# Kernel tuning notes

Hardware: AMD Instinct MI355X
Metric: run time of the kernel (lower is better)

Reference implementation:

```python
import jax, jax.numpy as jnp
import numpy as np

BATCH, IN, HID, OUT = 4096, 1024, 2048, 1000
ITERS = 50
LR = 0.001


def setup_inputs() -> dict:
    key = jax.random.key(0)
    k1, k2, k3 = jax.random.split(key, 3)
    x = jax.random.uniform(k1, (BATCH, IN), dtype=jnp.float32)
    # xavier_uniform for W_rec [HID, IN] and W_out [OUT, HID]
    lim_rec = float(np.sqrt(6.0 / (HID + IN)))
    lim_out = float(np.sqrt(6.0 / (OUT + HID)))
    W_rec = jax.random.uniform(k2, (HID, IN), minval=-lim_rec, maxval=lim_rec, dtype=jnp.float32)
    W_out = jax.random.uniform(k3, (OUT, HID), minval=-lim_out, maxval=lim_out, dtype=jnp.float32)
    bias_out = jnp.zeros((OUT,), dtype=jnp.float32)
    bias_gen = jnp.zeros((IN,), dtype=jnp.float32)
    return {"x": x, "W_rec": W_rec, "W_out": W_out, "bias_out": bias_out, "bias_gen": bias_gen}


def reference(x, W_rec, W_out, bias_out, bias_gen):
    batch = x.shape[0]
    h0 = jnp.zeros((batch, HID), dtype=x.dtype)
    y0 = jnp.zeros((batch, OUT), dtype=x.dtype)

    def step(carry, _):
        h, y, total_e = carry
        # generative prediction of input: sigmoid(h @ W_rec + bias_gen) [B, IN]
        x_pred = jax.nn.sigmoid(jnp.matmul(h, W_rec) + bias_gen)
        e_x = x - x_pred
        h = h + LR * jnp.matmul(e_x, W_rec.T)          # [B, HID]
        y_pred = jnp.matmul(h, W_out.T) + bias_out     # [B, OUT]
        e_y = y - y_pred
        y = y + LR * e_y
        energy = jnp.mean(jnp.sum(e_x * e_x, axis=1)) + jnp.mean(jnp.sum(e_y * e_y, axis=1))
        return (h, y, total_e + energy), None

    (h, y, total_energy), _ = jax.lax.scan(step, (h0, y0, jnp.float32(0.0)), None, length=ITERS)
    average_energy = total_energy / ITERS
    return y, average_energy
```

## Files before the change

### kernel.cpp

```cpp
#include <hip/hip_runtime.h>
#include <hip/hip_bf16.h>
#include <cstdint>

typedef __bf16 bf16_t;
typedef __bf16 bf16x4 __attribute__((ext_vector_type(4)));
typedef __bf16 bf16x8 __attribute__((ext_vector_type(8)));
typedef float f32x4 __attribute__((ext_vector_type(4)));

#define BATCH 4096
#define DIN   1024
#define HID   2048
#define DOUT  1000
#define NITER 50
#define LR    0.001f

#define BM 128
#define BN 128
#define BK 32
#define NBUF 4

#define GLDS(g, l)                                                        \
    __builtin_amdgcn_global_load_lds(                                     \
        (const __attribute__((address_space(1))) void*)(g),               \
        (__attribute__((address_space(3))) void*)(l), 16, 0, 0)

#define WAITVM(N) asm volatile("s_waitcnt vmcnt(" #N ")" ::: "memory")
#define BAR()     __builtin_amdgcn_s_barrier()
#define SCHEDB()  __builtin_amdgcn_sched_barrier(0)

template <int MODE>
__global__ __launch_bounds__(512) void pc_gemm(
    const bf16_t* __restrict__ Aex, bf16_t* __restrict__ wrecT,
    bf16_t* __restrict__ woutP, bf16_t* __restrict__ wg,
    bf16_t* __restrict__ wc,
    const float* __restrict__ xin, const float* __restrict__ bias_g,
    const float* __restrict__ bias_o,
    bf16_t* __restrict__ exnext, float* __restrict__ u,
    float* __restrict__ z, bf16_t* __restrict__ ey,
    float* __restrict__ yout, float* __restrict__ energy)
{
    __shared__ __align__(16) bf16_t sA[NBUF][BM * BK];
    __shared__ __align__(16) bf16_t sB[NBUF][BN * BK];
    __shared__ float red[8];

    const int t    = threadIdx.x;
    const int lane = t & 63;
    const int wave = t >> 6;
    const int wm   = wave >> 2;
    const int wn   = wave & 3;
    const int m0   = blockIdx.x * BM;
    const int lr   = lane & 15;
    const int lkb  = (lane >> 4) * 8;

    int role, n0, K;
    const bf16_t *Aop, *Bop;
    if constexpr (MODE == 3) {
        role = (int)blockIdx.y >= 8; n0 = ((int)blockIdx.y & 7) * BN; K = HID;
        Aop = role ? woutP : wrecT;  Bop = wrecT;
    } else if constexpr (MODE == 2) {
        role = 1; n0 = (int)blockIdx.y * BN; K = DIN;
        Aop = Aex; Bop = wc;
    } else {
        role = (int)blockIdx.y >= 8; n0 = ((int)blockIdx.y & 7) * BN; K = DIN;
        Aop = Aex; Bop = role ? wc : wg;
    }

    f32x4 acc[4][2] = {};

    const int srow = wave * 16 + (lane >> 2);
    const int scol = (lane & 3) * 8;
    const bf16_t* gA = Aop + (int64_t)(m0 + srow) * K + scol;
    const bf16_t* gB = Bop + (int64_t)(n0 + srow) * K + scol;

    auto stage = [&](int tile, int buf) {
        const int64_t ko = (int64_t)tile * BK;
        GLDS(gA + ko, &sA[buf][wave * 512]);
        GLDS(gB + ko, &sB[buf][wave * 512]);
    };

    auto compute = [&](int buf) {
        bf16x8 af[4], bfr[2];
#pragma unroll
        for (int mi = 0; mi < 4; ++mi)
            af[mi] = *reinterpret_cast<const bf16x8*>(
                &sA[buf][(wm * 64 + mi * 16 + lr) * BK + lkb]);
#pragma unroll
        for (int ni = 0; ni < 2; ++ni)
            bfr[ni] = *reinterpret_cast<const bf16x8*>(
                &sB[buf][(wn * 32 + ni * 16 + lr) * BK + lkb]);
#pragma unroll
        for (int mi = 0; mi < 4; ++mi)
#pragma unroll
            for (int ni = 0; ni < 2; ++ni)
                acc[mi][ni] = __builtin_amdgcn_mfma_f32_16x16x32_bf16(
                    af[mi], bfr[ni], acc[mi][ni], 0, 0, 0);
    };

    const int npairs = (K / BK) / 2;
    stage(0, 0); stage(1, 1); stage(2, 2); stage(3, 3);

    for (int p = 0; p < npairs - 2; ++p) {
        const int t0 = 2 * p;
        WAITVM(4);
        BAR();
        SCHEDB();
        compute(t0 & 3);
        compute((t0 + 1) & 3);
        BAR();
        stage(t0 + 4, t0 & 3);
        stage(t0 + 5, (t0 + 1) & 3);
    }
    {
        const int t0 = 2 * npairs - 4;
        WAITVM(4); BAR(); SCHEDB();
        compute(t0 & 3); compute((t0 + 1) & 3);
    }
    {
        const int t0 = 2 * npairs - 2;
        WAITVM(0); BAR(); SCHEDB();
        compute(t0 & 3); compute((t0 + 1) & 3);
    }

    float esum = 0.0f;
    const int prow = (lane >> 4) * 4;
#pragma unroll
    for (int mi = 0; mi < 4; ++mi) {
#pragma unroll
        for (int ni = 0; ni < 2; ++ni) {
            const int col = n0 + wn * 32 + ni * 16 + lr;
#pragma unroll
            for (int j = 0; j < 4; ++j) {
                const int row = m0 + wm * 64 + mi * 16 + prow + j;
                const float v = acc[mi][ni][j];
                if constexpr (MODE == 3) {
                    bf16_t* cout = role ? wc : wg;
                    cout[(int64_t)row * 1024 + col] = (bf16_t)v;
                } else {
                    if (role == 0) {
                        const int64_t idx = (int64_t)row * DIN + col;
                        const float D  = LR * v;
                        const float un = (MODE == 1 ? bias_g[col] : u[idx]) + D;
                        u[idx] = un;
                        const float xp = 1.0f / (1.0f + __expf(-un));
                        const float e  = xin[idx] - xp;
                        exnext[idx] = (bf16_t)e;
                        esum += e * e;
                    } else if (col < DOUT) {
                        const int64_t idx = (int64_t)row * 1024 + col;
                        const float D  = LR * v;
                        const float zn = (MODE == 1 ? bias_o[col] : z[idx]) + D;
                        const float eyn = (MODE == 1)
                            ? -zn
                            : (1.0f + LR) * (float)ey[idx] - D;
                        if constexpr (MODE == 2) {
                            yout[(int64_t)row * DOUT + col] =
                                (1.0f + LR) * eyn + zn;
                        } else {
                            z[idx]  = zn;
                            ey[idx] = (bf16_t)eyn;
                        }
                        esum += eyn * eyn;
                    }
                }
            }
        }
    }
    if constexpr (MODE != 3) {
#pragma unroll
        for (int off = 32; off; off >>= 1) esum += __shfl_down(esum, off, 64);
        if (lane == 0) red[wave] = esum;
        __syncthreads();
        if (t == 0) {
            float s = 0.0f;
#pragma unroll
            for (int w = 0; w < 8; ++w) s += red[w];
            atomicAdd(energy, s);
        }
    }
}

__global__ void conv_wrec(const float* __restrict__ W, bf16_t* __restrict__ WbT)
{
    __shared__ float tile[32][33];
    const int tx = threadIdx.x & 31;
    const int ty = threadIdx.x >> 5;
    const int c0 = blockIdx.x * 32;
    const int r0 = blockIdx.y * 32;
#pragma unroll
    for (int rr = ty; rr < 32; rr += 8)
        tile[rr][tx] = W[(int64_t)(r0 + rr) * DIN + c0 + tx];
    __syncthreads();
#pragma unroll
    for (int rr = ty; rr < 32; rr += 8)
        WbT[(int64_t)(c0 + rr) * HID + r0 + tx] = (bf16_t)tile[tx][rr];
}

__global__ void conv_wout(const float* __restrict__ W, bf16_t* __restrict__ Wb)
{
    const int i = blockIdx.x * 256 + threadIdx.x;
    const int r = i >> 11;
    const int c = i & 2047;
    Wb[i] = (r < DOUT) ? (bf16_t)W[(int64_t)r * HID + c] : (bf16_t)0.0f;
}

__global__ void ex0_kernel(const float* __restrict__ x,
                           const float* __restrict__ bias_g,
                           bf16_t* __restrict__ ex, float* __restrict__ energy)
{
    __shared__ float red[4];
    const int t = threadIdx.x, lane = t & 63, wave = t >> 6;
    const int i = (blockIdx.x * 256 + t) * 4;
    const int c0 = i & (DIN - 1);
    const float4 v = *reinterpret_cast<const float4*>(&x[i]);
    float e[4];
    const float b0 = bias_g[c0], b1 = bias_g[c0 + 1],
                b2 = bias_g[c0 + 2], b3 = bias_g[c0 + 3];
    e[0] = v.x - 1.0f / (1.0f + __expf(-b0));
    e[1] = v.y - 1.0f / (1.0f + __expf(-b1));
    e[2] = v.z - 1.0f / (1.0f + __expf(-b2));
    e[3] = v.w - 1.0f / (1.0f + __expf(-b3));
    bf16x4 o = {(bf16_t)e[0], (bf16_t)e[1], (bf16_t)e[2], (bf16_t)e[3]};
    *reinterpret_cast<bf16x4*>(&ex[i]) = o;
    float esum = e[0]*e[0] + e[1]*e[1] + e[2]*e[2] + e[3]*e[3];
#pragma unroll
    for (int off = 32; off; off >>= 1) esum += __shfl_down(esum, off, 64);
    if (lane == 0) red[wave] = esum;
    __syncthreads();
    if (t == 0) atomicAdd(energy, red[0] + red[1] + red[2] + red[3]);
}

__global__ void finalize_kernel(const float* __restrict__ energy,
                                float* __restrict__ out)
{
    out[0] = energy[0] * (1.0f / ((float)BATCH * (float)NITER));
}

extern "C" void kernel_launch(void* const* d_in, const int* in_sizes, int n_in,
                              void* d_out, int out_size, void* d_ws, size_t ws_size,
                              hipStream_t stream)
{
    (void)in_sizes; (void)n_in; (void)out_size; (void)ws_size;
    const float* x        = (const float*)d_in[0];
    const float* W_rec    = (const float*)d_in[1];
    const float* W_out    = (const float*)d_in[2];
    const float* bias_out = (const float*)d_in[3];
    const float* bias_gen = (const float*)d_in[4];
    float* y = (float*)d_out;

    char* ws = (char*)d_ws;
    size_t off = 0;
    float* u      = (float*)(ws + off);   off += (size_t)BATCH * DIN * 4;
    float* z      = (float*)(ws + off);   off += (size_t)BATCH * 1024 * 4;
    bf16_t* exA   = (bf16_t*)(ws + off);  off += (size_t)BATCH * DIN * 2;
    bf16_t* exB   = (bf16_t*)(ws + off);  off += (size_t)BATCH * DIN * 2;
    bf16_t* ey    = (bf16_t*)(ws + off);  off += (size_t)BATCH * 1024 * 2;
    bf16_t* wrecT = (bf16_t*)(ws + off);  off += (size_t)DIN * HID * 2;
    bf16_t* woutP = (bf16_t*)(ws + off);  off += (size_t)1024 * HID * 2;
    bf16_t* wg    = (bf16_t*)(ws + off);  off += (size_t)1024 * 1024 * 2;
    bf16_t* wc    = (bf16_t*)(ws + off);  off += (size_t)1024 * 1024 * 2;
    float* energy = (float*)(ws + off);   off += 256;

    hipMemsetAsync(energy, 0, 4, stream);

    conv_wrec<<<dim3(DIN / 32, HID / 32), 256, 0, stream>>>(W_rec, wrecT);
    conv_wout<<<(1024 * HID) / 256, 256, 0, stream>>>(W_out, woutP);
    pc_gemm<3><<<dim3(8, 16), 512, 0, stream>>>(
        nullptr, wrecT, woutP, wg, wc, nullptr, nullptr, nullptr,
        nullptr, nullptr, nullptr, nullptr, nullptr, nullptr);

    ex0_kernel<<<(BATCH * DIN) / 1024, 256, 0, stream>>>(x, bias_gen, exA, energy);

    bf16_t* exbuf[2] = {exA, exB};
    for (int it = 0; it < NITER; ++it) {
        const bf16_t* src = exbuf[it & 1];
        bf16_t* dst = exbuf[(it & 1) ^ 1];
        if (it == 0)
            pc_gemm<1><<<dim3(BATCH / BM, 16), 512, 0, stream>>>(
                src, nullptr, nullptr, wg, wc, x, bias_gen, bias_out,
                dst, u, z, ey, nullptr, energy);
        else if (it < NITER - 1)
            pc_gemm<0><<<dim3(BATCH / BM, 16), 512, 0, stream>>>(
                src, nullptr, nullptr, wg, wc, x, bias_gen, bias_out,
                dst, u, z, ey, nullptr, energy);
        else
            pc_gemm<2><<<dim3(BATCH / BM, 8), 512, 0, stream>>>(
                src, nullptr, nullptr, wg, wc, x, bias_gen, bias_out,
                nullptr, u, z, ey, y, energy);
    }
    finalize_kernel<<<1, 1, 0, stream>>>(energy, y + (size_t)BATCH * DOUT);
}
```

Baseline: 2.020 ms.

## Fuse all iterations into one persistent kernel with per-row-block barriers

```diff
diff --git a/kernel.cpp b/kernel.cpp
--- a/kernel.cpp
+++ b/kernel.cpp
@@ -28,20 +28,197 @@
 #define BAR()     __builtin_amdgcn_s_barrier()
 #define SCHEDB()  __builtin_amdgcn_sched_barrier(0)
 
-template <int MODE>
-__global__ __launch_bounds__(512) void pc_gemm(
-    const bf16_t* __restrict__ Aex, bf16_t* __restrict__ wrecT,
-    bf16_t* __restrict__ woutP, bf16_t* __restrict__ wg,
-    bf16_t* __restrict__ wc,
+__device__ __forceinline__ unsigned int bf16_bits(float f) {
+    bf16_t h = (bf16_t)f;
+    unsigned short s;
+    __builtin_memcpy(&s, &h, 2);
+    return (unsigned int)s;
+}
+__device__ __forceinline__ float bf16_val(unsigned short s) {
+    unsigned int u = (unsigned int)s << 16;
+    float f;
+    __builtin_memcpy(&f, &u, 4);
+    return f;
+}
+
+__global__ __launch_bounds__(512, 2) void pc_persist(
+    bf16_t* __restrict__ exA, bf16_t* __restrict__ exB,
+    const bf16_t* __restrict__ wg, const bf16_t* __restrict__ wc,
     const float* __restrict__ xin, const float* __restrict__ bias_g,
     const float* __restrict__ bias_o,
-    bf16_t* __restrict__ exnext, float* __restrict__ u,
-    float* __restrict__ z, bf16_t* __restrict__ ey,
-    float* __restrict__ yout, float* __restrict__ energy)
+    float* __restrict__ yout, float* __restrict__ energy,
+    unsigned int* __restrict__ barcnt)
+{
+    __shared__ __align__(16) bf16_t sA [NBUF][BM * BK];
+    __shared__ __align__(16) bf16_t sBU[NBUF][BN * BK];
+    __shared__ __align__(16) bf16_t sBZ[NBUF][BN * BK];
+    __shared__ float red[8];
+
+    const int t    = threadIdx.x;
+    const int lane = t & 63;
+    const int wave = t >> 6;
+    const int wm   = wave >> 2;
+    const int wn   = wave & 3;
+    const int m    = blockIdx.x >> 3;
+    const int n    = blockIdx.x & 7;
+    const int m0   = m * BM;
+    const int n0   = n * BN;
+    const int lr   = lane & 15;
+    const int lkb  = (lane >> 4) * 8;
+    const int prow = (lane >> 4) * 4;
+
+    const int srow = wave * 16 + (lane >> 2);
+    const int scol = (lane & 3) * 8;
+    const bf16_t* gBu = wg + (int64_t)(n0 + srow) * DIN + scol;
+    const bf16_t* gBz = wc + (int64_t)(n0 + srow) * DIN + scol;
+
+    float uSt[4][2][4];
+    float zSt[4][2][4];
+    unsigned int eyp[4][2][2];
+    float esum = 0.0f;
+
+    const bf16_t* Asrc = exA;
+    bf16_t*       Adst = exB;
+
+    for (int it = 0; it < NITER; ++it) {
+        const bf16_t* gA = Asrc + (int64_t)(m0 + srow) * DIN + scol;
+        f32x4 accU[4][2] = {};
+        f32x4 accZ[4][2] = {};
+
+        auto stage = [&](int tile, int buf) {
+            const int64_t ko = (int64_t)tile * BK;
+            GLDS(gA  + ko, &sA [buf][wave * 512]);
+            GLDS(gBu + ko, &sBU[buf][wave * 512]);
+            GLDS(gBz + ko, &sBZ[buf][wave * 512]);
+        };
+        auto compute = [&](int buf) {
+            bf16x8 af[4], bu[2], bz[2];
+#pragma unroll
+            for (int mi = 0; mi < 4; ++mi)
+                af[mi] = *reinterpret_cast<const bf16x8*>(
+                    &sA[buf][(wm * 64 + mi * 16 + lr) * BK + lkb]);
+#pragma unroll
+            for (int ni = 0; ni < 2; ++ni) {
+                bu[ni] = *reinterpret_cast<const bf16x8*>(
+                    &sBU[buf][(wn * 32 + ni * 16 + lr) * BK + lkb]);
+                bz[ni] = *reinterpret_cast<const bf16x8*>(
+                    &sBZ[buf][(wn * 32 + ni * 16 + lr) * BK + lkb]);
+            }
+#pragma unroll
+            for (int mi = 0; mi < 4; ++mi)
+#pragma unroll
+                for (int ni = 0; ni < 2; ++ni) {
+                    accU[mi][ni] = __builtin_amdgcn_mfma_f32_16x16x32_bf16(
+                        af[mi], bu[ni], accU[mi][ni], 0, 0, 0);
+                    accZ[mi][ni] = __builtin_amdgcn_mfma_f32_16x16x32_bf16(
+                        af[mi], bz[ni], accZ[mi][ni], 0, 0, 0);
+                }
+        };
+
+        const int npairs = (DIN / BK) / 2;
+        stage(0, 0); stage(1, 1); stage(2, 2); stage(3, 3);
+        for (int p = 0; p < npairs - 2; ++p) {
+            const int t0 = 2 * p;
+            WAITVM(6);
+            BAR();
+            SCHEDB();
+            compute(t0 & 3);
+            compute((t0 + 1) & 3);
+            BAR();
+            stage(t0 + 4, t0 & 3);
+            stage(t0 + 5, (t0 + 1) & 3);
+        }
+        {
+            const int t0 = 2 * npairs - 4;
+            WAITVM(6); BAR(); SCHEDB();
+            compute(t0 & 3); compute((t0 + 1) & 3);
+        }
+        {
+            const int t0 = 2 * npairs - 2;
+            WAITVM(0); BAR(); SCHEDB();
+            compute(t0 & 3); compute((t0 + 1) & 3);
+        }
+
+#pragma unroll
+        for (int mi = 0; mi < 4; ++mi) {
+#pragma unroll
+            for (int ni = 0; ni < 2; ++ni) {
+                const int col = n0 + wn * 32 + ni * 16 + lr;
+#pragma unroll
+                for (int j = 0; j < 4; ++j) {
+                    const int row = m0 + wm * 64 + mi * 16 + prow + j;
+                    if (it != NITER - 1) {
+                        const int64_t idx = (int64_t)row * DIN + col;
+                        const float D = LR * accU[mi][ni][j];
+                        const float base = (it == 0) ? bias_g[col]
+                                                     : uSt[mi][ni][j];
+                        const float un = base + D;
+                        uSt[mi][ni][j] = un;
+                        const float xp = 1.0f / (1.0f + __expf(-un));
+                        const float e  = xin[idx] - xp;
+                        Adst[idx] = (bf16_t)e;
+                        esum += e * e;
+                    }
+                    if (col < DOUT) {
+                        const float D = LR * accZ[mi][ni][j];
+                        const float base = (it == 0) ? bias_o[col]
+                                                     : zSt[mi][ni][j];
+                        const float zn = base + D;
+                        zSt[mi][ni][j] = zn;
+                        const unsigned int w = eyp[mi][ni][j >> 1];
+                        const float eyold = bf16_val(
+                            (j & 1) ? (unsigned short)(w >> 16)
+                                    : (unsigned short)(w & 0xFFFFu));
+                        const float eyn =
+                            (it == 0) ? -zn : (1.0f + LR) * eyold - D;
+                        if (it == NITER - 1) {
+                            yout[(int64_t)row * DOUT + col] =
+                                (1.0f + LR) * eyn + zn;
+                        } else {
+                            const unsigned int b = bf16_bits(eyn);
+                            eyp[mi][ni][j >> 1] =
+                                (j & 1) ? ((w & 0x0000FFFFu) | (b << 16))
+                                        : ((w & 0xFFFF0000u) | b);
+                        }
+                        esum += eyn * eyn;
+                    }
+                }
+            }
+        }
+
+        if (it != NITER - 1) {
+            __syncthreads();
+            if (t == 0) {
+                __threadfence();
+                atomicAdd(&barcnt[m], 1u);
+                const unsigned int tgt = 8u * (unsigned int)(it + 1);
+                while (atomicAdd(&barcnt[m], 0u) < tgt)
+                    __builtin_amdgcn_s_sleep(8);
+                __threadfence();
+            }
+            __syncthreads();
+        }
+        bf16_t* tmp = Adst; Adst = (bf16_t*)Asrc; Asrc = tmp;
+    }
+
+#pragma unroll
+    for (int off = 32; off; off >>= 1) esum += __shfl_down(esum, off, 64);
+    if (lane == 0) red[wave] = esum;
+    __syncthreads();
+    if (t == 0) {
+        float s = 0.0f;
+#pragma unroll
+        for (int w = 0; w < 8; ++w) s += red[w];
+        atomicAdd(energy, s);
+    }
+}
+
+__global__ __launch_bounds__(512) void setup_gemm(
+    const bf16_t* __restrict__ wrecT, const bf16_t* __restrict__ woutP,
+    bf16_t* __restrict__ wg, bf16_t* __restrict__ wc)
 {
     __shared__ __align__(16) bf16_t sA[NBUF][BM * BK];
     __shared__ __align__(16) bf16_t sB[NBUF][BN * BK];
-    __shared__ float red[8];
 
     const int t    = threadIdx.x;
     const int lane = t & 63;
@@ -49,35 +226,24 @@
     const int wm   = wave >> 2;
     const int wn   = wave & 3;
     const int m0   = blockIdx.x * BM;
+    const int role = (int)blockIdx.y >= 8;
+    const int n0   = ((int)blockIdx.y & 7) * BN;
     const int lr   = lane & 15;
     const int lkb  = (lane >> 4) * 8;
-
-    int role, n0, K;
-    const bf16_t *Aop, *Bop;
-    if constexpr (MODE == 3) {
-        role = (int)blockIdx.y >= 8; n0 = ((int)blockIdx.y & 7) * BN; K = HID;
-        Aop = role ? woutP : wrecT;  Bop = wrecT;
-    } else if constexpr (MODE == 2) {
-        role = 1; n0 = (int)blockIdx.y * BN; K = DIN;
-        Aop = Aex; Bop = wc;
-    } else {
-        role = (int)blockIdx.y >= 8; n0 = ((int)blockIdx.y & 7) * BN; K = DIN;
-        Aop = Aex; Bop = role ? wc : wg;
-    }
+    const int prow = (lane >> 4) * 4;
 
     f32x4 acc[4][2] = {};
 
     const int srow = wave * 16 + (lane >> 2);
     const int scol = (lane & 3) * 8;
-    const bf16_t* gA = Aop + (int64_t)(m0 + srow) * K + scol;
-    const bf16_t* gB = Bop + (int64_t)(n0 + srow) * K + scol;
+    const bf16_t* gA = (role ? woutP : wrecT) + (int64_t)(m0 + srow) * HID + scol;
+    const bf16_t* gB = wrecT + (int64_t)(n0 + srow) * HID + scol;
 
     auto stage = [&](int tile, int buf) {
         const int64_t ko = (int64_t)tile * BK;
         GLDS(gA + ko, &sA[buf][wave * 512]);
         GLDS(gB + ko, &sB[buf][wave * 512]);
     };
-
     auto compute = [&](int buf) {
         bf16x8 af[4], bfr[2];
 #pragma unroll
@@ -96,19 +262,14 @@
                     af[mi], bfr[ni], acc[mi][ni], 0, 0, 0);
     };
 
-    const int npairs = (K / BK) / 2;
+    const int npairs = (HID / BK) / 2;
     stage(0, 0); stage(1, 1); stage(2, 2); stage(3, 3);
-
     for (int p = 0; p < npairs - 2; ++p) {
         const int t0 = 2 * p;
-        WAITVM(4);
+        WAITVM(4); BAR(); SCHEDB();
+        compute(t0 & 3); compute((t0 + 1) & 3);
         BAR();
-        SCHEDB();
-        compute(t0 & 3);
-        compute((t0 + 1) & 3);
-        BAR();
-        stage(t0 + 4, t0 & 3);
-        stage(t0 + 5, (t0 + 1) & 3);
+        stage(t0 + 4, t0 & 3); stage(t0 + 5, (t0 + 1) & 3);
     }
     {
         const int t0 = 2 * npairs - 4;
@@ -121,62 +282,18 @@
         compute(t0 & 3); compute((t0 + 1) & 3);
     }
 
-    float esum = 0.0f;
-    const int prow = (lane >> 4) * 4;
-#pragma unroll
-    for (int mi = 0; mi < 4; ++mi) {
+    bf16_t* cout = role ? wc : wg;
+#pragma unroll
+    for (int mi = 0; mi < 4; ++mi)
 #pragma unroll
         for (int ni = 0; ni < 2; ++ni) {
             const int col = n0 + wn * 32 + ni * 16 + lr;
 #pragma unroll
             for (int j = 0; j < 4; ++j) {
                 const int row = m0 + wm * 64 + mi * 16 + prow + j;
-                const float v = acc[mi][ni][j];
-                if constexpr (MODE == 3) {
-                    bf16_t* cout = role ? wc : wg;
-                    cout[(int64_t)row * 1024 + col] = (bf16_t)v;
-                } else {
-                    if (role == 0) {
-                        const int64_t idx = (int64_t)row * DIN + col;
-                        const float D  = LR * v;
-                        const float un = (MODE == 1 ? bias_g[col] : u[idx]) + D;
-                        u[idx] = un;
-                        const float xp = 1.0f / (1.0f + __expf(-un));
-                        const float e  = xin[idx] - xp;
-                        exnext[idx] = (bf16_t)e;
-                        esum += e * e;
-                    } else if (col < DOUT) {
-                        const int64_t idx = (int64_t)row * 1024 + col;
-                        const float D  = LR * v;
-                        const float zn = (MODE == 1 ? bias_o[col] : z[idx]) + D;
-                        const float eyn = (MODE == 1)
-                            ? -zn
-                            : (1.0f + LR) * (float)ey[idx] - D;
-                        if constexpr (MODE == 2) {
-                            yout[(int64_t)row * DOUT + col] =
-                                (1.0f + LR) * eyn + zn;
-                        } else {
-                            z[idx]  = zn;
-                            ey[idx] = (bf16_t)eyn;
-                        }
-                        esum += eyn * eyn;
-                    }
-                }
+                cout[(int64_t)row * 1024 + col] = (bf16_t)acc[mi][ni][j];
             }
         }
-    }
-    if constexpr (MODE != 3) {
-#pragma unroll
-        for (int off = 32; off; off >>= 1) esum += __shfl_down(esum, off, 64);
-        if (lane == 0) red[wave] = esum;
-        __syncthreads();
-        if (t == 0) {
-            float s = 0.0f;
-#pragma unroll
-            for (int w = 0; w < 8; ++w) s += red[w];
-            atomicAdd(energy, s);
-        }
-    }
 }
 
 __global__ void conv_wrec(const float* __restrict__ W, bf16_t* __restrict__ WbT)
@@ -249,43 +366,24 @@
 
     char* ws = (char*)d_ws;
     size_t off = 0;
-    float* u      = (float*)(ws + off);   off += (size_t)BATCH * DIN * 4;
-    float* z      = (float*)(ws + off);   off += (size_t)BATCH * 1024 * 4;
     bf16_t* exA   = (bf16_t*)(ws + off);  off += (size_t)BATCH * DIN * 2;
     bf16_t* exB   = (bf16_t*)(ws + off);  off += (size_t)BATCH * DIN * 2;
-    bf16_t* ey    = (bf16_t*)(ws + off);  off += (size_t)BATCH * 1024 * 2;
     bf16_t* wrecT = (bf16_t*)(ws + off);  off += (size_t)DIN * HID * 2;
     bf16_t* woutP = (bf16_t*)(ws + off);  off += (size_t)1024 * HID * 2;
     bf16_t* wg    = (bf16_t*)(ws + off);  off += (size_t)1024 * 1024 * 2;
     bf16_t* wc    = (bf16_t*)(ws + off);  off += (size_t)1024 * 1024 * 2;
-    float* energy = (float*)(ws + off);   off += 256;
-
-    hipMemsetAsync(energy, 0, 4, stream);
+    float* energy = (float*)(ws + off);
+    unsigned int* barcnt = (unsigned int*)(ws + off + 64);
+
+    hipMemsetAsync(energy, 0, 256, stream);
 
     conv_wrec<<<dim3(DIN / 32, HID / 32), 256, 0, stream>>>(W_rec, wrecT);
     conv_wout<<<(1024 * HID) / 256, 256, 0, stream>>>(W_out, woutP);
-    pc_gemm<3><<<dim3(8, 16), 512, 0, stream>>>(
-        nullptr, wrecT, woutP, wg, wc, nullptr, nullptr, nullptr,
-        nullptr, nullptr, nullptr, nullptr, nullptr, nullptr);
-
+    setup_gemm<<<dim3(8, 16), 512, 0, stream>>>(wrecT, woutP, wg, wc);
     ex0_kernel<<<(BATCH * DIN) / 1024, 256, 0, stream>>>(x, bias_gen, exA, energy);
 
-    bf16_t* exbuf[2] = {exA, exB};
-    for (int it = 0; it < NITER; ++it) {
-        const bf16_t* src = exbuf[it & 1];
-        bf16_t* dst = exbuf[(it & 1) ^ 1];
-        if (it == 0)
-            pc_gemm<1><<<dim3(BATCH / BM, 16), 512, 0, stream>>>(
-                src, nullptr, nullptr, wg, wc, x, bias_gen, bias_out,
-                dst, u, z, ey, nullptr, energy);
-        else if (it < NITER - 1)
-            pc_gemm<0><<<dim3(BATCH / BM, 16), 512, 0, stream>>>(
-                src, nullptr, nullptr, wg, wc, x, bias_gen, bias_out,
-                dst, u, z, ey, nullptr, energy);
-        else
-            pc_gemm<2><<<dim3(BATCH / BM, 8), 512, 0, stream>>>(
-                src, nullptr, nullptr, wg, wc, x, bias_gen, bias_out,
-                nullptr, u, z, ey, y, energy);
-    }
+    pc_persist<<<dim3(256), dim3(512), 0, stream>>>(
+        exA, exB, wg, wc, x, bias_gen, bias_out, y, energy, barcnt);
+
     finalize_kernel<<<1, 1, 0, stream>>>(energy, y + (size_t)BATCH * DOUT);
 }
```

After: 2.841 ms. 1.41x slower.
